# Kernel optimization log

Hardware: AMD Instinct MI355X
Metric: run time of the kernel (lower is better)

The kernel has to match this reference:

```python
import jax, jax.numpy as jnp
import numpy as np

S, D = 4096, 512


def setup_inputs() -> dict:
    key = jax.random.key(0)
    ks = jax.random.split(key, 10)
    names = ['x', 'w_ql', 'w_kl', 'w_qr', 'w_kr', 'w_qg', 'w_kg', 'w_qloc', 'w_kloc', 'w_v']
    shapes = [(S, D)] + [(D, D)] * 9
    scale = [1.0] + [float(np.sqrt(2.0 / (D + D)))] * 9  # xavier-ish for weights
    return {n: jax.random.normal(k, sh, dtype=jnp.float32) * s
            for n, k, sh, s in zip(names, ks, shapes, scale)}


def reference(x, w_ql, w_kl, w_qr, w_kr, w_qg, w_kg, w_qloc, w_kloc, w_v):
    # x: [S, D]
    s, d = x.shape
    norm = jnp.sqrt(jnp.asarray(d, x.dtype))
    # strict upper triangle (j > i) is masked for the left boundary,
    # strict lower triangle (i > j) for the right boundary
    mask_up = jnp.triu(jnp.ones((s, s), dtype=bool), k=1)

    ql, kl = x @ w_ql, x @ w_kl
    qr, kr = x @ w_qr, x @ w_kr

    neg_inf = jnp.asarray(-jnp.inf, x.dtype)
    left_scores = jnp.where(mask_up, neg_inf, ql @ kl.T) / norm            # [S,S]
    left_boundary = jax.nn.softmax(left_scores, axis=1)
    right_scores = jnp.where(mask_up.T, neg_inf, qr @ kr.T) / norm
    right_boundary = jax.nn.softmax(right_scores, axis=1)

    # left_boundary @ triu(ones)  == forward cumsum along columns
    # right_boundary @ tril(ones) == reverse cumsum along columns
    left_cdf = jnp.cumsum(left_boundary, axis=1)
    right_cdf = jnp.cumsum(right_boundary[:, ::-1], axis=1)[:, ::-1]
    att_mask = left_cdf * right_cdf                                        # [S,S]

    s_glb = (x @ w_qg) @ (x @ w_kg).T                                      # [S,S]
    s_loc = ((x @ w_qloc) @ (x @ w_kloc).T) * att_mask                     # additive local path
    score = (s_glb + s_loc) / norm

    att_weight = jax.nn.softmax(score, axis=1)
    att_output = att_weight @ (x @ w_v)                                    # [S,D]
    return att_output, att_weight
```

## Files before the change

### kernel.cpp

```cpp
#include <hip/hip_runtime.h>


#define SS 4096
#define DD 512
#define INV_NORM 0.04419417382415922f

typedef _Float16 f16;
typedef f16 f16x8 __attribute__((ext_vector_type(8)));
typedef f16 f16x4 __attribute__((ext_vector_type(4)));
typedef float f32x4 __attribute__((ext_vector_type(4)));
typedef unsigned short ushort;
typedef ushort ushort4v __attribute__((ext_vector_type(4)));

#define GAS __attribute__((address_space(1)))
#define LAS __attribute__((address_space(3)))

#define BARM() asm volatile("s_barrier" ::: "memory")
#define WAITV(N) asm volatile("s_waitcnt vmcnt(" #N ")" ::: "memory")

__device__ __forceinline__ void ldsdma16(const void* g, void* l) {
  __builtin_amdgcn_global_load_lds((const GAS void*)g, (LAS void*)l, 16, 0, 0);
}

__device__ __forceinline__ ushort f2bf(float f) {
  unsigned u = __float_as_uint(f);
  return (ushort)((u + 0x7FFFu + ((u >> 16) & 1u)) >> 16);
}
__device__ __forceinline__ float bf2f(ushort h) {
  return __uint_as_float((unsigned)h << 16);
}

__device__ __forceinline__ void stage16(const f16* __restrict__ src, int ldk, f16* lds, int k0) {
  const int tid  = threadIdx.x;
  const int lane = tid & 63;
  const int wv   = tid >> 6;
  const int rb   = wv * 8 + (lane >> 3);
  const int cs   = lane & 7;
#pragma unroll
  for (int c = 0; c < 4; ++c) {
    const int r = c * 32 + rb;
    const int q = cs ^ (r & 7);
    ldsdma16(src + (size_t)r * ldk + k0 + q * 8, lds + c * 2048 + wv * 512);
  }
}

__device__ __forceinline__ f16x8 fragld(const f16* lds, int r0, int qb) {
  const int lane = threadIdx.x & 63;
  const int r = r0 + (lane & 15);
  const int q = (qb + (lane >> 4)) ^ (r & 7);
  return *(const f16x8*)(lds + r * 64 + q * 8);
}

__device__ __forceinline__ void mma64(const f16* As, const f16* Bs, f32x4 acc[2][8]) {
  const int wv = threadIdx.x >> 6;
#pragma unroll
  for (int ks = 0; ks < 2; ++ks) {
    const f16x8 a0 = fragld(As, wv * 32,      ks * 4);
    const f16x8 a1 = fragld(As, wv * 32 + 16, ks * 4);
#pragma unroll
    for (int j = 0; j < 8; ++j) {
      const f16x8 b = fragld(Bs, j * 16, ks * 4);
      acc[0][j] = __builtin_amdgcn_mfma_f32_16x16x32_f16(a0, b, acc[0][j], 0, 0, 0);
      acc[1][j] = __builtin_amdgcn_mfma_f32_16x16x32_f16(a1, b, acc[1][j], 0, 0, 0);
    }
  }
}

__global__ void k_prep(const float* __restrict__ x, const float* w0, const float* w1,
                       const float* w2, const float* w3, const float* w4, const float* w5,
                       const float* w6, const float* w7, const float* w8,
                       f16* __restrict__ xh, f16* __restrict__ wt) {
  const int bx = blockIdx.x;
  if (bx < 2048) {
    const size_t i = ((size_t)bx * 256 + threadIdx.x) * 4;
    const float4 f = *(const float4*)(x + i);
    f16x4 h = { (f16)f.x, (f16)f.y, (f16)f.z, (f16)f.w };
    *(f16x4*)(xh + i) = h;
    return;
  }
  const int idx = bx - 2048;
  const int bz = idx >> 8;
  const int rem = idx & 255;
  const int n0 = (rem & 15) * 32, k0 = (rem >> 4) * 32;
  const float* srcs[9] = {w0, w1, w2, w3, w4, w5, w6, w7, w8};
  const float* src = srcs[bz];
  f16* dst = wt + (size_t)bz * DD * DD;
  __shared__ float t[32][33];
  const int tx = threadIdx.x & 31, ty = threadIdx.x >> 5;
#pragma unroll
  for (int i = 0; i < 32; i += 8)
    t[ty + i][tx] = src[(size_t)(k0 + ty + i) * DD + n0 + tx];
  __syncthreads();
#pragma unroll
  for (int i = 0; i < 32; i += 8)
    dst[(size_t)(n0 + ty + i) * DD + k0 + tx] = (f16)t[tx][ty + i];
}

__global__ __launch_bounds__(256, 3) void k_proj(const f16* __restrict__ xh,
                                                 const f16* __restrict__ wt,
                                                 f16* __restrict__ proj,
                                                 f16* __restrict__ vt) {
  __shared__ __align__(16) f16 As[8192];
  __shared__ __align__(16) f16 Bs[8192];
  const int z = blockIdx.z;
  const f16* B = wt + (size_t)z * DD * DD;
  f16* C = proj + (size_t)z * SS * DD;
  const int R0 = blockIdx.y * 128, C0 = blockIdx.x * 128;
  f32x4 acc[2][8];
#pragma unroll
  for (int i = 0; i < 2; ++i)
#pragma unroll
    for (int j = 0; j < 8; ++j) acc[i][j] = (f32x4){0.f, 0.f, 0.f, 0.f};
  for (int kb = 0; kb < DD / 64; ++kb) {
    __syncthreads();
    stage16(xh + (size_t)R0 * DD, DD, As, kb * 64);
    stage16(B  + (size_t)C0 * DD, DD, Bs, kb * 64);
    __syncthreads();
    mma64(As, Bs, acc);
  }
  const int lane = threadIdx.x & 63, wv = threadIdx.x >> 6;
  const int mm = lane & 15, quad = lane >> 4;
#pragma unroll
  for (int i = 0; i < 2; ++i)
#pragma unroll
    for (int j = 0; j < 8; ++j)
#pragma unroll
      for (int r = 0; r < 4; ++r)
        C[(size_t)(R0 + wv * 32 + i * 16 + quad * 4 + r) * DD + C0 + j * 16 + mm] =
            (f16)acc[i][j][r];
  if (z == 8) {
#pragma unroll
    for (int i = 0; i < 2; ++i)
#pragma unroll
      for (int j = 0; j < 8; ++j)
#pragma unroll
        for (int r = 0; r < 4; ++r)
          vt[(size_t)(C0 + j * 16 + mm) * SS + (R0 + wv * 32 + i * 16 + quad * 4 + r)] =
              (f16)acc[i][j][r];
  }
}

__global__ __launch_bounds__(256, 3) void k_bnd(const f16* __restrict__ proj,
                                                f16* __restrict__ eL,
                                                f16* __restrict__ eR) {
  const int t = blockIdx.x, dir = blockIdx.y;
  int rbk = (int)((sqrtf(8.f * t + 1.f) - 1.f) * 0.5f);
  while ((rbk + 1) * (rbk + 2) / 2 <= t) ++rbk;
  while (rbk * (rbk + 1) / 2 > t) --rbk;
  int jt = t - rbk * (rbk + 1) / 2;
  if (dir) { jt = 31 - jt; rbk = 31 - rbk; }
  __shared__ __align__(16) f16 As[8192];
  __shared__ __align__(16) f16 Bs[8192];
  const f16* q  = proj + (size_t)(dir ? 2 : 0) * SS * DD;
  const f16* kp = proj + (size_t)(dir ? 3 : 1) * SS * DD;
  const int R0 = rbk * 128, C0 = jt * 128;
  f32x4 acc[2][8];
#pragma unroll
  for (int i = 0; i < 2; ++i)
#pragma unroll
    for (int j = 0; j < 8; ++j) acc[i][j] = (f32x4){0.f, 0.f, 0.f, 0.f};
  for (int kb = 0; kb < DD / 64; ++kb) {
    __syncthreads();
    stage16(q  + (size_t)R0 * DD, DD, As, kb * 64);
    stage16(kp + (size_t)C0 * DD, DD, Bs, kb * 64);
    __syncthreads();
    mma64(As, Bs, acc);
  }
  const int lane = threadIdx.x & 63, wv = threadIdx.x >> 6;
  const int mm = lane & 15, quad = lane >> 4;
  const bool diag = (jt == rbk);
  f16* outp = dir ? eR : eL;
#pragma unroll
  for (int i = 0; i < 2; ++i)
#pragma unroll
    for (int r = 0; r < 4; ++r) {
      const int rl = wv * 32 + i * 16 + quad * 4 + r;
#pragma unroll
      for (int j = 0; j < 8; ++j) {
        const int cl = j * 16 + mm;
        const float sc = acc[i][j][r] * INV_NORM;
        const bool bad = diag && (dir ? (cl < rl) : (cl > rl));
        const float e = bad ? 0.f : __expf(sc);
        outp[(size_t)(R0 + rl) * SS + (C0 + cl)] = (f16)e;
      }
    }
}

__global__ __launch_bounds__(1024) void k_cumsum(f16* __restrict__ eL,
                                                 const f16* __restrict__ eR) {
  const int i = blockIdx.x;
  const int tid = threadIdx.x, lane = tid & 63, wv = tid >> 6;
  __shared__ float wsL[16], wsR[16];
  const int j0 = tid * 4;

  float pl[4] = {0.f, 0.f, 0.f, 0.f};
  if (j0 <= i) {
    const f16x4 hl = *(const f16x4*)(eL + (size_t)i * SS + j0);
#pragma unroll
    for (int u = 0; u < 4; ++u) pl[u] = (j0 + u <= i) ? (float)hl[u] : 0.f;
  }
#pragma unroll
  for (int u = 1; u < 4; ++u) pl[u] += pl[u - 1];
  const float Tl = pl[3];
  float sl = Tl;
#pragma unroll
  for (int d = 1; d < 64; d <<= 1) {
    const float o = __shfl_up(sl, (unsigned)d, 64);
    if (lane >= d) sl += o;
  }
  if (lane == 63) wsL[wv] = sl;

  float rr[4] = {0.f, 0.f, 0.f, 0.f}, pr[4];
  if (j0 + 3 >= i) {
    const f16x4 hr = *(const f16x4*)(eR + (size_t)i * SS + j0);
#pragma unroll
    for (int u = 0; u < 4; ++u) rr[u] = (j0 + u >= i) ? (float)hr[u] : 0.f;
  }
  pr[0] = rr[0];
#pragma unroll
  for (int u = 1; u < 4; ++u) pr[u] = pr[u - 1] + rr[u];
  const float Tr = pr[3];
  float sr = Tr;
#pragma unroll
  for (int d = 1; d < 64; d <<= 1) {
    const float o = __shfl_up(sr, (unsigned)d, 64);
    if (lane >= d) sr += o;
  }
  if (lane == 63) wsR[wv] = sr;

  __syncthreads();
  float offL = 0.f, totL = 0.f, offR = 0.f, totR = 0.f;
#pragma unroll
  for (int ww = 0; ww < 16; ++ww) {
    const float a = wsL[ww], b = wsR[ww];
    if (ww < wv) { offL += a; offR += b; }
    totL += a; totR += b;
  }
  const float exL = offL + sl - Tl;
  const float exR = offR + sr - Tr;
  const float invL = 1.f / totL, invR = 1.f / totR;

  f16x4 out;
#pragma unroll
  for (int u = 0; u < 4; ++u) {
    const int j = j0 + u;
    const float cdfL = (exL + pl[u]) * invL;
    const float pre  = exR + pr[u];
    const float cdfR = (totR - pre + rr[u]) * invR;
    const float m = (j < i) ? cdfL : ((j > i) ? cdfR : 1.f);
    out[u] = (f16)m;
  }
  *(f16x4*)(eL + (size_t)i * SS + j0) = out;
}

__device__ __forceinline__ float mask_ld(const f16* Am, const f16* Bm, int r, int c) {
  const f16* b = (c < 64) ? Am : Bm;
  const int cc = c & 63;
  const int q = (cc >> 3) ^ (r & 7);
  return (float)b[r * 64 + q * 8 + (cc & 7)];
}

__global__ __launch_bounds__(256, 2) void k_score(const f16* __restrict__ proj,
                                                  const f16* __restrict__ mask,
                                                  f16* __restrict__ ehalf,
                                                  float* __restrict__ lsc) {
  __shared__ __align__(16) f16 Ag[8192];
  __shared__ __align__(16) f16 Bg[8192];
  __shared__ __align__(16) f16 Al[8192];
  __shared__ __align__(16) f16 Bl[8192];
  const int jt = blockIdx.x, rbk = blockIdx.y;
  const f16* qg = proj + (size_t)4 * SS * DD;
  const f16* kg = proj + (size_t)5 * SS * DD;
  const f16* ql = proj + (size_t)6 * SS * DD;
  const f16* kl = proj + (size_t)7 * SS * DD;
  const int R0 = rbk * 128, C0 = jt * 128;
  f32x4 ag[2][8], al[2][8];
#pragma unroll
  for (int i = 0; i < 2; ++i)
#pragma unroll
    for (int j = 0; j < 8; ++j) {
      ag[i][j] = (f32x4){0.f, 0.f, 0.f, 0.f};
      al[i][j] = (f32x4){0.f, 0.f, 0.f, 0.f};
    }
  stage16(qg + (size_t)R0 * DD, DD, Ag, 0);
  stage16(kg + (size_t)C0 * DD, DD, Bg, 0);
  stage16(ql + (size_t)R0 * DD, DD, Al, 0);
  stage16(kl + (size_t)C0 * DD, DD, Bl, 0);
  for (int kb = 0; kb < DD / 64 - 1; ++kb) {
    WAITV(8);
    BARM();
    __builtin_amdgcn_s_setprio(1);
    mma64(Ag, Bg, ag);
    __builtin_amdgcn_s_setprio(0);
    BARM();
    stage16(qg + (size_t)R0 * DD, DD, Ag, kb * 64 + 64);
    stage16(kg + (size_t)C0 * DD, DD, Bg, kb * 64 + 64);
    WAITV(8);
    BARM();
    __builtin_amdgcn_s_setprio(1);
    mma64(Al, Bl, al);
    __builtin_amdgcn_s_setprio(0);
    BARM();
    stage16(ql + (size_t)R0 * DD, DD, Al, kb * 64 + 64);
    stage16(kl + (size_t)C0 * DD, DD, Bl, kb * 64 + 64);
  }
  WAITV(8);
  BARM();
  __builtin_amdgcn_s_setprio(1);
  mma64(Ag, Bg, ag);
  __builtin_amdgcn_s_setprio(0);
  BARM();
  stage16(mask + (size_t)R0 * SS, SS, Ag, C0);
  stage16(mask + (size_t)R0 * SS, SS, Bg, C0 + 64);
  WAITV(8);
  BARM();
  __builtin_amdgcn_s_setprio(1);
  mma64(Al, Bl, al);
  __builtin_amdgcn_s_setprio(0);
  WAITV(0);
  BARM();

  const int lane = threadIdx.x & 63, wv = threadIdx.x >> 6;
  const int mm = lane & 15, quad = lane >> 4;
  float ls[2][4];
#pragma unroll
  for (int i = 0; i < 2; ++i)
#pragma unroll
    for (int r = 0; r < 4; ++r) ls[i][r] = 0.f;
#pragma unroll
  for (int i = 0; i < 2; ++i)
#pragma unroll
    for (int r = 0; r < 4; ++r) {
      const int rl = wv * 32 + i * 16 + quad * 4 + r;
      const int rg = R0 + rl;
#pragma unroll
      for (int j = 0; j < 8; ++j) {
        const int cl = j * 16 + mm;
        const float mk = mask_ld(Ag, Bg, rl, cl);
        const float scv = (ag[i][j][r] + al[i][j][r] * mk) * INV_NORM;
        const float e = __expf(scv);
        ehalf[(size_t)rg * SS + (C0 + cl)] = (f16)e;
        ls[i][r] += e;
      }
    }
#pragma unroll
  for (int d = 1; d < 16; d <<= 1)
#pragma unroll
    for (int i = 0; i < 2; ++i)
#pragma unroll
      for (int r = 0; r < 4; ++r)
        ls[i][r] += __shfl_xor(ls[i][r], d, 64);
  if (mm == 0) {
#pragma unroll
    for (int i = 0; i < 2; ++i)
#pragma unroll
      for (int r = 0; r < 4; ++r)
        atomicAdd(&lsc[R0 + wv * 32 + i * 16 + quad * 4 + r], ls[i][r]);
  }
}

__global__ __launch_bounds__(256, 4) void k_pv(const f16* __restrict__ ehalf,
                                               const f16* __restrict__ vt,
                                               ushort* __restrict__ part) {
  __shared__ __align__(16) f16 As[8192];
  __shared__ __align__(16) f16 Bs[8192];
  const int C0 = blockIdx.x * 128, R0 = blockIdx.y * 128, zk = blockIdx.z;
  f32x4 acc[2][8];
#pragma unroll
  for (int i = 0; i < 2; ++i)
#pragma unroll
    for (int j = 0; j < 8; ++j) acc[i][j] = (f32x4){0.f, 0.f, 0.f, 0.f};
  for (int kb = 0; kb < 16; ++kb) {
    const int k0 = zk * 1024 + kb * 64;
    __syncthreads();
    stage16(ehalf + (size_t)R0 * SS, SS, As, k0);
    stage16(vt    + (size_t)C0 * SS, SS, Bs, k0);
    __syncthreads();
    mma64(As, Bs, acc);
  }
  const int lane = threadIdx.x & 63, wv = threadIdx.x >> 6;
  const int mm = lane & 15, quad = lane >> 4;
  ushort* P = part + (size_t)zk * SS * DD;
#pragma unroll
  for (int i = 0; i < 2; ++i)
#pragma unroll
    for (int j = 0; j < 8; ++j)
#pragma unroll
      for (int r = 0; r < 4; ++r)
        P[(size_t)(R0 + wv * 32 + i * 16 + quad * 4 + r) * DD + C0 + j * 16 + mm] =
            f2bf(acc[i][j][r]);
}

__global__ void k_fin(const f16* __restrict__ ehalf, const ushort* __restrict__ part,
                      const float* __restrict__ lsc, float* __restrict__ outw,
                      float* __restrict__ O) {
  const int bx = blockIdx.x;
  if (bx < 8192) {
    const size_t idx = ((size_t)bx * 256 + threadIdx.x) * 8;
    const int row = (int)(idx >> 12);
    const float inv = 1.f / lsc[row];
    const f16x8 h = *(const f16x8*)(ehalf + idx);
    float4 a = { (float)h[0] * inv, (float)h[1] * inv, (float)h[2] * inv, (float)h[3] * inv };
    float4 b = { (float)h[4] * inv, (float)h[5] * inv, (float)h[6] * inv, (float)h[7] * inv };
    *(float4*)(outw + idx) = a;
    *(float4*)(outw + idx + 4) = b;
  } else {
    const size_t idx = ((size_t)(bx - 8192) * 256 + threadIdx.x) * 4;
    const int row = (int)(idx >> 9);
    float s0 = 0.f, s1 = 0.f, s2 = 0.f, s3 = 0.f;
#pragma unroll
    for (int p = 0; p < 4; ++p) {
      const ushort4v v = *(const ushort4v*)(part + (size_t)p * SS * DD + idx);
      s0 += bf2f(v[0]); s1 += bf2f(v[1]); s2 += bf2f(v[2]); s3 += bf2f(v[3]);
    }
    const float inv = 1.f / lsc[row];
    float4 s = { s0 * inv, s1 * inv, s2 * inv, s3 * inv };
    *(float4*)(O + idx) = s;
  }
}

extern "C" void kernel_launch(void* const* d_in, const int* in_sizes, int n_in,
                              void* d_out, int out_size, void* d_ws, size_t ws_size,
                              hipStream_t stream) {
  (void)in_sizes; (void)n_in; (void)out_size; (void)ws_size;
  const float* x = (const float*)d_in[0];
  const float* w[9];
  for (int i = 0; i < 9; ++i) w[i] = (const float*)d_in[1 + i];
  float* O    = (float*)d_out;
  float* outw = O + (size_t)SS * DD;

  char* ws = (char*)d_ws;
  size_t off = 0;
  auto alloc = [&](size_t b) { void* p = ws + off; off += (b + 255) & ~(size_t)255; return p; };
  f16* xh     = (f16*)alloc((size_t)SS * DD * 2);
  f16* wt     = (f16*)alloc((size_t)9 * DD * DD * 2);
  f16* proj   = (f16*)alloc((size_t)9 * SS * DD * 2);
  f16* vt     = (f16*)alloc((size_t)DD * SS * 2);
  f16* eL     = (f16*)alloc((size_t)SS * SS * 2);
  f16* eR     = (f16*)alloc((size_t)SS * SS * 2);
  f16* ehalf  = (f16*)alloc((size_t)SS * SS * 2);
  float* lsc  = (float*)alloc((size_t)SS * 4);
  ushort* part = (ushort*)eR;

  hipMemsetAsync(lsc, 0, (size_t)SS * 4, stream);
  k_prep<<<4352, 256, 0, stream>>>(x, w[0], w[1], w[2], w[3], w[4], w[5], w[6], w[7], w[8],
                                   xh, wt);
  k_proj<<<dim3(4, 32, 9), 256, 0, stream>>>(xh, wt, proj, vt);
  k_bnd<<<dim3(528, 2), 256, 0, stream>>>(proj, eL, eR);
  k_cumsum<<<SS, 1024, 0, stream>>>(eL, eR);
  k_score<<<dim3(32, 32), 256, 0, stream>>>(proj, eL, ehalf, lsc);
  k_pv<<<dim3(4, 32, 4), 256, 0, stream>>>(ehalf, vt, part);
  k_fin<<<10240, 256, 0, stream>>>(ehalf, part, lsc, outw, O);
}
```

Measured before the change: 290.0 us.

## Double-buffer LDS staging in projection, boundary and PV GEMM kernels

Replaces the single-buffer sync/stage/sync/mma loops in k_proj, k_bnd and k_pv with a two-stage ping-pong LDS pipeline. Async global-to-LDS loads for the next K-slice are issued while the current slice is multiplied, with vmcnt waits replacing full __syncthreads. This doubles LDS per block, so launch bounds drop to 2 blocks per CU, trading occupancy for overlap of loads with compute. It also removes the s_setprio priority bumps from the fused score kernel.

```diff
diff --git a/kernel.cpp b/kernel.cpp
--- a/kernel.cpp
+++ b/kernel.cpp
@@ -96,28 +96,43 @@
     dst[(size_t)(n0 + ty + i) * DD + k0 + tx] = (f16)t[tx][ty + i];
 }
 
-__global__ __launch_bounds__(256, 3) void k_proj(const f16* __restrict__ xh,
+__global__ __launch_bounds__(256, 2) void k_proj(const f16* __restrict__ xh,
                                                  const f16* __restrict__ wt,
                                                  f16* __restrict__ proj,
                                                  f16* __restrict__ vt) {
-  __shared__ __align__(16) f16 As[8192];
-  __shared__ __align__(16) f16 Bs[8192];
+  __shared__ __align__(16) f16 As[2][8192];
+  __shared__ __align__(16) f16 Bs[2][8192];
   const int z = blockIdx.z;
   const f16* B = wt + (size_t)z * DD * DD;
   f16* C = proj + (size_t)z * SS * DD;
   const int R0 = blockIdx.y * 128, C0 = blockIdx.x * 128;
+  const f16* Ap = xh + (size_t)R0 * DD;
+  const f16* Bp = B + (size_t)C0 * DD;
   f32x4 acc[2][8];
 #pragma unroll
   for (int i = 0; i < 2; ++i)
 #pragma unroll
     for (int j = 0; j < 8; ++j) acc[i][j] = (f32x4){0.f, 0.f, 0.f, 0.f};
-  for (int kb = 0; kb < DD / 64; ++kb) {
-    __syncthreads();
-    stage16(xh + (size_t)R0 * DD, DD, As, kb * 64);
-    stage16(B  + (size_t)C0 * DD, DD, Bs, kb * 64);
-    __syncthreads();
-    mma64(As, Bs, acc);
-  }
+  stage16(Ap, DD, As[0], 0);
+  stage16(Bp, DD, Bs[0], 0);
+  stage16(Ap, DD, As[1], 64);
+  stage16(Bp, DD, Bs[1], 64);
+  for (int kb = 0; kb < 6; kb += 2) {
+    WAITV(8); BARM();
+    mma64(As[0], Bs[0], acc);
+    BARM();
+    stage16(Ap, DD, As[0], (kb + 2) * 64);
+    stage16(Bp, DD, Bs[0], (kb + 2) * 64);
+    WAITV(8); BARM();
+    mma64(As[1], Bs[1], acc);
+    BARM();
+    stage16(Ap, DD, As[1], (kb + 3) * 64);
+    stage16(Bp, DD, Bs[1], (kb + 3) * 64);
+  }
+  WAITV(8); BARM();
+  mma64(As[0], Bs[0], acc);
+  WAITV(0); BARM();
+  mma64(As[1], Bs[1], acc);
   const int lane = threadIdx.x & 63, wv = threadIdx.x >> 6;
   const int mm = lane & 15, quad = lane >> 4;
 #pragma unroll
@@ -140,7 +155,7 @@
   }
 }
 
-__global__ __launch_bounds__(256, 3) void k_bnd(const f16* __restrict__ proj,
+__global__ __launch_bounds__(256, 2) void k_bnd(const f16* __restrict__ proj,
                                                 f16* __restrict__ eL,
                                                 f16* __restrict__ eR) {
   const int t = blockIdx.x, dir = blockIdx.y;
@@ -149,23 +164,38 @@
   while (rbk * (rbk + 1) / 2 > t) --rbk;
   int jt = t - rbk * (rbk + 1) / 2;
   if (dir) { jt = 31 - jt; rbk = 31 - rbk; }
-  __shared__ __align__(16) f16 As[8192];
-  __shared__ __align__(16) f16 Bs[8192];
+  __shared__ __align__(16) f16 As[2][8192];
+  __shared__ __align__(16) f16 Bs[2][8192];
   const f16* q  = proj + (size_t)(dir ? 2 : 0) * SS * DD;
   const f16* kp = proj + (size_t)(dir ? 3 : 1) * SS * DD;
   const int R0 = rbk * 128, C0 = jt * 128;
+  const f16* Ap = q + (size_t)R0 * DD;
+  const f16* Bp = kp + (size_t)C0 * DD;
   f32x4 acc[2][8];
 #pragma unroll
   for (int i = 0; i < 2; ++i)
 #pragma unroll
     for (int j = 0; j < 8; ++j) acc[i][j] = (f32x4){0.f, 0.f, 0.f, 0.f};
-  for (int kb = 0; kb < DD / 64; ++kb) {
-    __syncthreads();
-    stage16(q  + (size_t)R0 * DD, DD, As, kb * 64);
-    stage16(kp + (size_t)C0 * DD, DD, Bs, kb * 64);
-    __syncthreads();
-    mma64(As, Bs, acc);
-  }
+  stage16(Ap, DD, As[0], 0);
+  stage16(Bp, DD, Bs[0], 0);
+  stage16(Ap, DD, As[1], 64);
+  stage16(Bp, DD, Bs[1], 64);
+  for (int kb = 0; kb < 6; kb += 2) {
+    WAITV(8); BARM();
+    mma64(As[0], Bs[0], acc);
+    BARM();
+    stage16(Ap, DD, As[0], (kb + 2) * 64);
+    stage16(Bp, DD, Bs[0], (kb + 2) * 64);
+    WAITV(8); BARM();
+    mma64(As[1], Bs[1], acc);
+    BARM();
+    stage16(Ap, DD, As[1], (kb + 3) * 64);
+    stage16(Bp, DD, Bs[1], (kb + 3) * 64);
+  }
+  WAITV(8); BARM();
+  mma64(As[0], Bs[0], acc);
+  WAITV(0); BARM();
+  mma64(As[1], Bs[1], acc);
   const int lane = threadIdx.x & 63, wv = threadIdx.x >> 6;
   const int mm = lane & 15, quad = lane >> 4;
   const bool diag = (jt == rbk);
@@ -289,34 +319,26 @@
   for (int kb = 0; kb < DD / 64 - 1; ++kb) {
     WAITV(8);
     BARM();
-    __builtin_amdgcn_s_setprio(1);
     mma64(Ag, Bg, ag);
-    __builtin_amdgcn_s_setprio(0);
     BARM();
     stage16(qg + (size_t)R0 * DD, DD, Ag, kb * 64 + 64);
     stage16(kg + (size_t)C0 * DD, DD, Bg, kb * 64 + 64);
     WAITV(8);
     BARM();
-    __builtin_amdgcn_s_setprio(1);
     mma64(Al, Bl, al);
-    __builtin_amdgcn_s_setprio(0);
     BARM();
     stage16(ql + (size_t)R0 * DD, DD, Al, kb * 64 + 64);
     stage16(kl + (size_t)C0 * DD, DD, Bl, kb * 64 + 64);
   }
   WAITV(8);
   BARM();
-  __builtin_amdgcn_s_setprio(1);
   mma64(Ag, Bg, ag);
-  __builtin_amdgcn_s_setprio(0);
   BARM();
   stage16(mask + (size_t)R0 * SS, SS, Ag, C0);
   stage16(mask + (size_t)R0 * SS, SS, Bg, C0 + 64);
   WAITV(8);
   BARM();
-  __builtin_amdgcn_s_setprio(1);
   mma64(Al, Bl, al);
-  __builtin_amdgcn_s_setprio(0);
   WAITV(0);
   BARM();
 
@@ -359,25 +381,40 @@
   }
 }
 
-__global__ __launch_bounds__(256, 4) void k_pv(const f16* __restrict__ ehalf,
+__global__ __launch_bounds__(256, 2) void k_pv(const f16* __restrict__ ehalf,
                                                const f16* __restrict__ vt,
                                                ushort* __restrict__ part) {
-  __shared__ __align__(16) f16 As[8192];
-  __shared__ __align__(16) f16 Bs[8192];
+  __shared__ __align__(16) f16 As[2][8192];
+  __shared__ __align__(16) f16 Bs[2][8192];
   const int C0 = blockIdx.x * 128, R0 = blockIdx.y * 128, zk = blockIdx.z;
+  const f16* Ap = ehalf + (size_t)R0 * SS;
+  const f16* Bp = vt + (size_t)C0 * SS;
+  const int kz = zk * 1024;
   f32x4 acc[2][8];
 #pragma unroll
   for (int i = 0; i < 2; ++i)
 #pragma unroll
     for (int j = 0; j < 8; ++j) acc[i][j] = (f32x4){0.f, 0.f, 0.f, 0.f};
-  for (int kb = 0; kb < 16; ++kb) {
-    const int k0 = zk * 1024 + kb * 64;
-    __syncthreads();
-    stage16(ehalf + (size_t)R0 * SS, SS, As, k0);
-    stage16(vt    + (size_t)C0 * SS, SS, Bs, k0);
-    __syncthreads();
-    mma64(As, Bs, acc);
-  }
+  stage16(Ap, SS, As[0], kz);
+  stage16(Bp, SS, Bs[0], kz);
+  stage16(Ap, SS, As[1], kz + 64);
+  stage16(Bp, SS, Bs[1], kz + 64);
+  for (int kb = 0; kb < 14; kb += 2) {
+    WAITV(8); BARM();
+    mma64(As[0], Bs[0], acc);
+    BARM();
+    stage16(Ap, SS, As[0], kz + (kb + 2) * 64);
+    stage16(Bp, SS, Bs[0], kz + (kb + 2) * 64);
+    WAITV(8); BARM();
+    mma64(As[1], Bs[1], acc);
+    BARM();
+    stage16(Ap, SS, As[1], kz + (kb + 3) * 64);
+    stage16(Bp, SS, Bs[1], kz + (kb + 3) * 64);
+  }
+  WAITV(8); BARM();
+  mma64(As[0], Bs[0], acc);
+  WAITV(0); BARM();
+  mma64(As[1], Bs[1], acc);
   const int lane = threadIdx.x & 63, wv = threadIdx.x >> 6;
   const int mm = lane & 15, quad = lane >> 4;
   ushort* P = part + (size_t)zk * SS * DD;
```

Result: no change. 290.4 us (+0.1%).
